# Kernel tuning notes

Measured on AMD Instinct MI355X. Metric: run time of the kernel, lower is better.

## Reference

```python
import jax, jax.numpy as jnp
import numpy as np

CAPACITY_FACTOR = 1.0


def _top1_gate(x2d, wg):
    """GShard-style top-1 switch gate.
    x2d: [S, m], wg: [m, E] -> (l_aux, combine [S,E,C], dispatch [S,E,C])
    """
    S, _ = x2d.shape
    E = wg.shape[1]
    C = int(CAPACITY_FACTOR * S / E)  # expert capacity
    logits = x2d @ wg                              # [S, E]
    gates = jax.nn.softmax(logits, axis=-1)        # [S, E]
    idx = jnp.argmax(gates, axis=-1)               # [S]
    mask = jax.nn.one_hot(idx, E, dtype=jnp.int32) # [S, E]
    loc = jnp.cumsum(mask, axis=0) - 1             # position within each expert
    # load-balancing aux loss
    me = jnp.mean(gates, axis=0)
    ce = jnp.mean(mask.astype(gates.dtype), axis=0)
    l_aux = E * jnp.sum(me * ce)
    # drop tokens over capacity
    mask = mask * (loc < C).astype(jnp.int32)
    gate_s = jnp.sum(gates * mask, axis=-1)        # [S] gate value of kept token
    loc_s = jnp.sum(loc * mask, axis=-1)           # [S] slot index
    loc_oh = jax.nn.one_hot(loc_s, C, dtype=gates.dtype)          # [S, C]
    combine = (gate_s[:, None] * mask.astype(gates.dtype))[:, :, None] * loc_oh[:, None, :]  # [S,E,C]
    dispatch = (combine > 0).astype(gates.dtype)
    return l_aux, combine, dispatch


def setup_inputs() -> dict:
    key = jax.random.key(0)
    k1, k2, k3, k4 = jax.random.split(key, 4)
    s, b, m, E, ffn = 2048, 4, 1024, 8, 4096
    x = jax.random.normal(k1, (s, b, m), dtype=jnp.float32)
    wg = jax.random.normal(k2, (m, E), dtype=jnp.float32) * 0.02
    w1 = jax.random.normal(k3, (E, m, ffn), dtype=jnp.float32) * 0.02
    w2 = jax.random.normal(k4, (E, ffn, m), dtype=jnp.float32) * 0.02
    return {"x": x, "wg": wg, "w1": w1, "w2": w2}


def reference(x, wg, w1, w2):
    # world_size = 1, num_local_experts = E, num_prototypes z = 1
    s, b, m = x.shape
    x2d = x.reshape(-1, m)                          # [S, m]
    l_aux, combine, dispatch = _top1_gate(x2d, wg)  # [S,E,C]
    combine = combine[:, None]                      # [S, z=1, E, C]
    dispatch = dispatch[:, None]
    xr = x2d[:, None, :]                            # [S, z=1, m]
    # dense dispatch: szfc,szm->zfcm
    dispatched = jnp.einsum('szfc,szm->zfcm', dispatch, xr)
    # all-to-all with world_size=1 is identity; reshape to [E, C, m]
    E = w1.shape[0]
    di = dispatched.reshape(E, -1, m)               # [E, C, m]
    # experts: per-expert FFN with ReLU
    h = jax.nn.relu(jnp.einsum('ecm,emh->ech', di, w1))
    eo = jnp.einsum('ech,ehm->ecm', h, w2)          # [E, C, m]
    eo = eo[None]                                   # [z=1, E, C, m]
    out = jnp.einsum('szfc,zfcm->sm', combine, eo)  # [S, m]
    return out.reshape(s, b, m)
```

## Files before the change

### kernel.cpp

```cpp
#include <hip/hip_runtime.h>
#include <hip/hip_bf16.h>


#define NTOK 8192
#define DM   1024
#define NE   8
#define NF   4096
#define CAP  1024

typedef __bf16 bf16x8 __attribute__((ext_vector_type(8)));
typedef float  f32x4  __attribute__((ext_vector_type(4)));

__device__ __forceinline__ unsigned short f2bf(float f) {
    union { float f; unsigned int u; } v; v.f = f;
    unsigned int u = v.u;
    return (unsigned short)((u + 0x7FFFu + ((u >> 16) & 1u)) >> 16);
}

__device__ __forceinline__ void async_cp16(const unsigned short* g, unsigned short* l) {
    __builtin_amdgcn_global_load_lds(
        (const __attribute__((address_space(1))) void*)g,
        (__attribute__((address_space(3))) void*)l, 16, 0, 0);
}

__global__ __launch_bounds__(256) void gate_kernel(
    const float* __restrict__ x, const float* __restrict__ wg,
    int* __restrict__ eid, float* __restrict__ gatev)
{
    int wave = threadIdx.x >> 6;
    int lane = threadIdx.x & 63;
    int t = blockIdx.x * 4 + wave;
    const float* xr = x + (size_t)t * DM;
    float acc[NE];
#pragma unroll
    for (int e = 0; e < NE; ++e) acc[e] = 0.f;
    for (int k = lane; k < DM; k += 64) {
        float xv = xr[k];
        const float4* wr = (const float4*)(wg + k * NE);
        float4 w0 = wr[0], w1 = wr[1];
        acc[0] += xv * w0.x; acc[1] += xv * w0.y;
        acc[2] += xv * w0.z; acc[3] += xv * w0.w;
        acc[4] += xv * w1.x; acc[5] += xv * w1.y;
        acc[6] += xv * w1.z; acc[7] += xv * w1.w;
    }
#pragma unroll
    for (int off = 32; off >= 1; off >>= 1) {
#pragma unroll
        for (int e = 0; e < NE; ++e) acc[e] += __shfl_xor(acc[e], off, 64);
    }
    if (lane == 0) {
        int best = 0; float bm = acc[0];
#pragma unroll
        for (int e = 1; e < NE; ++e) if (acc[e] > bm) { bm = acc[e]; best = e; }
        float ssum = 0.f;
#pragma unroll
        for (int e = 0; e < NE; ++e) ssum += __expf(acc[e] - bm);
        eid[t] = best;
        gatev[t] = 1.0f / ssum;
    }
}

__global__ __launch_bounds__(1024) void scan_kernel(
    const int* __restrict__ eid, int* __restrict__ slot_token)
{
    __shared__ int sc[1024][NE];
    int tid = threadIdx.x;
#pragma unroll
    for (int i = 0; i < 8; ++i) slot_token[tid + i * 1024] = -1;

    int e_loc[8];
    int cnt[NE];
#pragma unroll
    for (int e = 0; e < NE; ++e) cnt[e] = 0;
#pragma unroll
    for (int i = 0; i < 8; ++i) {
        int e = eid[tid * 8 + i];
        e_loc[i] = e;
        cnt[e]++;
    }
#pragma unroll
    for (int e = 0; e < NE; ++e) sc[tid][e] = cnt[e];
    __syncthreads();
    for (int stride = 1; stride < 1024; stride <<= 1) {
        int v[NE];
        if (tid >= stride) {
#pragma unroll
            for (int e = 0; e < NE; ++e) v[e] = sc[tid - stride][e];
        } else {
#pragma unroll
            for (int e = 0; e < NE; ++e) v[e] = 0;
        }
        __syncthreads();
#pragma unroll
        for (int e = 0; e < NE; ++e) sc[tid][e] += v[e];
        __syncthreads();
    }
    int off_[NE];
#pragma unroll
    for (int e = 0; e < NE; ++e) off_[e] = (tid == 0) ? 0 : sc[tid - 1][e];
#pragma unroll
    for (int i = 0; i < 8; ++i) {
        int e = e_loc[i];
        int loc = off_[e]++;
        if (loc < CAP) slot_token[e * CAP + loc] = tid * 8 + i;
    }
}

template<int K, int N>
__global__ __launch_bounds__(256) void convT_kernel(
    const float* __restrict__ W, unsigned short* __restrict__ WT)
{
    __shared__ unsigned short tile[64][66];
    int e = blockIdx.z;
    int k0 = blockIdx.y * 64, n0 = blockIdx.x * 64;
    const float* Wp = W + (size_t)e * K * N;
    unsigned short* WTp = WT + (size_t)e * K * N;
    int tid = threadIdx.x;
    int cn = (tid & 15) * 4;
    int rk = tid >> 4;
#pragma unroll
    for (int i = 0; i < 4; ++i) {
        int k = rk + i * 16;
        float4 v = *(const float4*)(Wp + (size_t)(k0 + k) * N + n0 + cn);
        tile[cn + 0][k] = f2bf(v.x);
        tile[cn + 1][k] = f2bf(v.y);
        tile[cn + 2][k] = f2bf(v.z);
        tile[cn + 3][k] = f2bf(v.w);
    }
    __syncthreads();
    int ck = (tid & 15) * 4;
    int rn = tid >> 4;
#pragma unroll
    for (int i = 0; i < 4; ++i) {
        int n = rn + i * 16;
        ushort4 o;
        o.x = tile[n][ck + 0]; o.y = tile[n][ck + 1];
        o.z = tile[n][ck + 2]; o.w = tile[n][ck + 3];
        *(ushort4*)(WTp + (size_t)(n0 + n) * K + k0 + ck) = o;
    }
}

__global__ __launch_bounds__(256) void gather_kernel(
    const float* __restrict__ x, const int* __restrict__ slot_token,
    unsigned short* __restrict__ Xd)
{
    int slot = blockIdx.x;
    int t = slot_token[slot];
    int c4 = threadIdx.x * 4;
    ushort4 o;
    if (t >= 0) {
        float4 v = *(const float4*)(x + (size_t)t * DM + c4);
        o.x = f2bf(v.x); o.y = f2bf(v.y); o.z = f2bf(v.z); o.w = f2bf(v.w);
    } else {
        o.x = 0; o.y = 0; o.z = 0; o.w = 0;
    }
    *(ushort4*)(Xd + (size_t)slot * DM + c4) = o;
}

template<int K>
__device__ __forceinline__ void gemm_core(
    const unsigned short* __restrict__ Ab, const unsigned short* __restrict__ Bb,
    unsigned short* As, unsigned short* Bs, f32x4 acc[4][4])
{
    int tid = threadIdx.x;
    int wave = tid >> 6, lane = tid & 63;
    int wr = (wave >> 1) * 64;
    int wc = (wave & 1) * 64;
#pragma unroll
    for (int i = 0; i < 4; ++i)
#pragma unroll
        for (int j = 0; j < 4; ++j) acc[i][j] = (f32x4){0.f, 0.f, 0.f, 0.f};

    int srow = (lane >> 2);
    int scol = (lane & 3) * 8;

    for (int kt = 0; kt < K; kt += 32) {
#pragma unroll
        for (int i = 0; i < 2; ++i) {
            int q = wave * 2 + i;
            int row = q * 16 + srow;
            const unsigned short* ga = Ab + (size_t)row * K + kt + scol;
            const unsigned short* gb = Bb + (size_t)row * K + kt + scol;
            async_cp16(ga, As + q * 512);
            async_cp16(gb, Bs + q * 512);
        }
        __syncthreads();
        bf16x8 af[4], bfr[4];
#pragma unroll
        for (int i = 0; i < 4; ++i) {
            int r = wr + i * 16 + (lane & 15);
            af[i] = *(const bf16x8*)(As + r * 32 + (lane >> 4) * 8);
        }
#pragma unroll
        for (int j = 0; j < 4; ++j) {
            int c = wc + j * 16 + (lane & 15);
            bfr[j] = *(const bf16x8*)(Bs + c * 32 + (lane >> 4) * 8);
        }
#pragma unroll
        for (int i = 0; i < 4; ++i)
#pragma unroll
            for (int j = 0; j < 4; ++j)
                acc[i][j] = __builtin_amdgcn_mfma_f32_16x16x32_bf16(af[i], bfr[j], acc[i][j], 0, 0, 0);
        __syncthreads();
    }
}

__global__ __launch_bounds__(256, 2) void gemm1_kernel(
    const unsigned short* __restrict__ Xd, const unsigned short* __restrict__ W1T,
    unsigned short* __restrict__ H)
{
    __shared__ unsigned short As[128 * 32];
    __shared__ unsigned short Bs[128 * 32];
    int e = blockIdx.z;
    const unsigned short* Ab = Xd + ((size_t)e * CAP + blockIdx.y * 128) * DM;
    const unsigned short* Bb = W1T + ((size_t)e * NF + blockIdx.x * 128) * DM;
    f32x4 acc[4][4];
    gemm_core<DM>(Ab, Bb, As, Bs, acc);

    int tid = threadIdx.x, wave = tid >> 6, lane = tid & 63;
    int wr = (wave >> 1) * 64, wc = (wave & 1) * 64;
    size_t Hbase = ((size_t)e * CAP + blockIdx.y * 128) * NF + blockIdx.x * 128;
#pragma unroll
    for (int i = 0; i < 4; ++i) {
#pragma unroll
        for (int j = 0; j < 4; ++j) {
            int col = wc + j * 16 + (lane & 15);
#pragma unroll
            for (int f = 0; f < 4; ++f) {
                int row = wr + i * 16 + (lane >> 4) * 4 + f;
                float v = acc[i][j][f];
                v = v > 0.f ? v : 0.f;
                H[Hbase + (size_t)row * NF + col] = f2bf(v);
            }
        }
    }
}

__global__ __launch_bounds__(256, 2) void gemm2_kernel(
    const unsigned short* __restrict__ H, const unsigned short* __restrict__ W2T,
    const int* __restrict__ slot_token, const float* __restrict__ gatev,
    float* __restrict__ out)
{
    __shared__ unsigned short As[128 * 32];
    __shared__ unsigned short Bs[128 * 32];
    int e = blockIdx.z;
    const unsigned short* Ab = H + ((size_t)e * CAP + blockIdx.y * 128) * NF;
    const unsigned short* Bb = W2T + ((size_t)e * DM + blockIdx.x * 128) * NF;
    f32x4 acc[4][4];
    gemm_core<NF>(Ab, Bb, As, Bs, acc);

    int tid = threadIdx.x, wave = tid >> 6, lane = tid & 63;
    int wr = (wave >> 1) * 64, wc = (wave & 1) * 64;
    int slot0 = e * CAP + blockIdx.y * 128;
#pragma unroll
    for (int i = 0; i < 4; ++i) {
        int rbase = wr + i * 16 + (lane >> 4) * 4;
#pragma unroll
        for (int f = 0; f < 4; ++f) {
            int row = rbase + f;
            int t = slot_token[slot0 + row];
            if (t >= 0) {
                float g = gatev[t];
#pragma unroll
                for (int j = 0; j < 4; ++j) {
                    int col = blockIdx.x * 128 + wc + j * 16 + (lane & 15);
                    out[(size_t)t * DM + col] = acc[i][j][f] * g;
                }
            }
        }
    }
}

extern "C" void kernel_launch(void* const* d_in, const int* in_sizes, int n_in,
                              void* d_out, int out_size, void* d_ws, size_t ws_size,
                              hipStream_t stream)
{
    const float* x  = (const float*)d_in[0];
    const float* wg = (const float*)d_in[1];
    const float* w1 = (const float*)d_in[2];
    const float* w2 = (const float*)d_in[3];
    float* out = (float*)d_out;

    char* ws = (char*)d_ws;
    size_t o = 0;
    auto nxt = [&](size_t b) { size_t r = o; o += (b + 255) & ~(size_t)255; return r; };
    int*   eid        = (int*)  (ws + nxt((size_t)NTOK * 4));
    float* gatev      = (float*)(ws + nxt((size_t)NTOK * 4));
    int*   slot_token = (int*)  (ws + nxt((size_t)NTOK * 4));
    unsigned short* Xd = (unsigned short*)(ws + nxt((size_t)NTOK * DM * 2));
    unsigned short* WT = (unsigned short*)(ws + nxt((size_t)NE * NF * DM * 2));
    unsigned short* Hb = (unsigned short*)(ws + nxt((size_t)NE * CAP * NF * 2));

    gate_kernel<<<NTOK / 4, 256, 0, stream>>>(x, wg, eid, gatev);
    scan_kernel<<<1, 1024, 0, stream>>>(eid, slot_token);
    convT_kernel<DM, NF><<<dim3(NF / 64, DM / 64, NE), 256, 0, stream>>>(w1, WT);
    gather_kernel<<<NTOK, 256, 0, stream>>>(x, slot_token, Xd);
    gemm1_kernel<<<dim3(NF / 128, CAP / 128, NE), 256, 0, stream>>>(Xd, WT, Hb);
    convT_kernel<NF, DM><<<dim3(DM / 64, NF / 64, NE), 256, 0, stream>>>(w2, WT);
    hipMemsetAsync(d_out, 0, (size_t)out_size * sizeof(float), stream);
    gemm2_kernel<<<dim3(DM / 128, CAP / 128, NE), 256, 0, stream>>>(Hb, WT, slot_token, gatev, out);
}
```

Measured before the change: 558.5 us.

## Retile gemm2, stage gemm1 epilogue through LDS, and vectorize gate/scan/gather/transpose

The gemm2 kernel moves to a 128x64 output tile with a K step of 64 and an occupancy hint of 4, launching twice as many blocks so more of the GPU is busy and fewer barriers are paid per K. The gemm1 epilogue writes ReLU'd bf16 into shared memory and then issues coalesced 16-byte stores, replacing scattered 2-byte global writes. The scan kernel switches from a shared-memory Hillis-Steele scan with many block barriers to a wavefront shuffle scan plus per-wave totals. The gate, gather and transpose kernels get wider vector loads and stores. Risks include LDS bank conflicts in the new layouts and a gemm2 tile that reuses B less per load.

```diff
diff --git a/kernel.cpp b/kernel.cpp
--- a/kernel.cpp
+++ b/kernel.cpp
@@ -10,6 +10,7 @@
 
 typedef __bf16 bf16x8 __attribute__((ext_vector_type(8)));
 typedef float  f32x4  __attribute__((ext_vector_type(4)));
+typedef unsigned short us8v __attribute__((ext_vector_type(8)));
 
 __device__ __forceinline__ unsigned short f2bf(float f) {
     union { float f; unsigned int u; } v; v.f = f;
@@ -30,18 +31,24 @@
     int wave = threadIdx.x >> 6;
     int lane = threadIdx.x & 63;
     int t = blockIdx.x * 4 + wave;
-    const float* xr = x + (size_t)t * DM;
+    const float4* xr4 = (const float4*)(x + (size_t)t * DM);
     float acc[NE];
 #pragma unroll
     for (int e = 0; e < NE; ++e) acc[e] = 0.f;
-    for (int k = lane; k < DM; k += 64) {
-        float xv = xr[k];
-        const float4* wr = (const float4*)(wg + k * NE);
-        float4 w0 = wr[0], w1 = wr[1];
-        acc[0] += xv * w0.x; acc[1] += xv * w0.y;
-        acc[2] += xv * w0.z; acc[3] += xv * w0.w;
-        acc[4] += xv * w1.x; acc[5] += xv * w1.y;
-        acc[6] += xv * w1.z; acc[7] += xv * w1.w;
+#pragma unroll
+    for (int it = 0; it < 4; ++it) {
+        int k4 = lane + it * 64;
+        float4 xv = xr4[k4];
+        float xc[4] = {xv.x, xv.y, xv.z, xv.w};
+#pragma unroll
+        for (int c = 0; c < 4; ++c) {
+            const float4* wr = (const float4*)(wg + (size_t)(k4 * 4 + c) * NE);
+            float4 w0 = wr[0], w1 = wr[1];
+            acc[0] += xc[c] * w0.x; acc[1] += xc[c] * w0.y;
+            acc[2] += xc[c] * w0.z; acc[3] += xc[c] * w0.w;
+            acc[4] += xc[c] * w1.x; acc[5] += xc[c] * w1.y;
+            acc[6] += xc[c] * w1.z; acc[7] += xc[c] * w1.w;
+        }
     }
 #pragma unroll
     for (int off = 32; off >= 1; off >>= 1) {
@@ -63,45 +70,49 @@
 __global__ __launch_bounds__(1024) void scan_kernel(
     const int* __restrict__ eid, int* __restrict__ slot_token)
 {
-    __shared__ int sc[1024][NE];
+    __shared__ int wtot[16][NE];
     int tid = threadIdx.x;
+    int lane = tid & 63, wv = tid >> 6;
 #pragma unroll
     for (int i = 0; i < 8; ++i) slot_token[tid + i * 1024] = -1;
 
-    int e_loc[8];
+    int el[8];
     int cnt[NE];
 #pragma unroll
     for (int e = 0; e < NE; ++e) cnt[e] = 0;
 #pragma unroll
     for (int i = 0; i < 8; ++i) {
         int e = eid[tid * 8 + i];
-        e_loc[i] = e;
+        el[i] = e;
         cnt[e]++;
     }
-#pragma unroll
-    for (int e = 0; e < NE; ++e) sc[tid][e] = cnt[e];
+    int incl[NE];
+#pragma unroll
+    for (int e = 0; e < NE; ++e) incl[e] = cnt[e];
+#pragma unroll
+    for (int off = 1; off <= 32; off <<= 1) {
+#pragma unroll
+        for (int e = 0; e < NE; ++e) {
+            int v = __shfl_up(incl[e], off, 64);
+            if (lane >= off) incl[e] += v;
+        }
+    }
+    if (lane == 63) {
+#pragma unroll
+        for (int e = 0; e < NE; ++e) wtot[wv][e] = incl[e];
+    }
     __syncthreads();
-    for (int stride = 1; stride < 1024; stride <<= 1) {
-        int v[NE];
-        if (tid >= stride) {
-#pragma unroll
-            for (int e = 0; e < NE; ++e) v[e] = sc[tid - stride][e];
-        } else {
-#pragma unroll
-            for (int e = 0; e < NE; ++e) v[e] = 0;
-        }
-        __syncthreads();
-#pragma unroll
-        for (int e = 0; e < NE; ++e) sc[tid][e] += v[e];
-        __syncthreads();
-    }
-    int off_[NE];
-#pragma unroll
-    for (int e = 0; e < NE; ++e) off_[e] = (tid == 0) ? 0 : sc[tid - 1][e];
+    int base[NE];
+#pragma unroll
+    for (int e = 0; e < NE; ++e) {
+        int s = 0;
+        for (int w = 0; w < 16; ++w) s += (w < wv) ? wtot[w][e] : 0;
+        base[e] = s + incl[e] - cnt[e];
+    }
 #pragma unroll
     for (int i = 0; i < 8; ++i) {
-        int e = e_loc[i];
-        int loc = off_[e]++;
+        int e = el[i];
+        int loc = base[e]++;
         if (loc < CAP) slot_token[e * CAP + loc] = tid * 8 + i;
     }
 }
@@ -110,7 +121,7 @@
 __global__ __launch_bounds__(256) void convT_kernel(
     const float* __restrict__ W, unsigned short* __restrict__ WT)
 {
-    __shared__ unsigned short tile[64][66];
+    __shared__ unsigned short tile[64][72];
     int e = blockIdx.z;
     int k0 = blockIdx.y * 64, n0 = blockIdx.x * 64;
     const float* Wp = W + (size_t)e * K * N;
@@ -128,15 +139,15 @@
         tile[cn + 3][k] = f2bf(v.w);
     }
     __syncthreads();
-    int ck = (tid & 15) * 4;
-    int rn = tid >> 4;
-#pragma unroll
-    for (int i = 0; i < 4; ++i) {
-        int n = rn + i * 16;
-        ushort4 o;
-        o.x = tile[n][ck + 0]; o.y = tile[n][ck + 1];
-        o.z = tile[n][ck + 2]; o.w = tile[n][ck + 3];
-        *(ushort4*)(WTp + (size_t)(n0 + n) * K + k0 + ck) = o;
+    int ck = (tid & 7) * 8;
+    int rn = tid >> 3;
+#pragma unroll
+    for (int i = 0; i < 2; ++i) {
+        int n = rn + i * 32;
+        us8v o;
+#pragma unroll
+        for (int c = 0; c < 8; ++c) o[c] = tile[n][ck + c];
+        *(us8v*)(WTp + (size_t)(n0 + n) * K + k0 + ck) = o;
     }
 }
 
@@ -144,17 +155,22 @@
     const float* __restrict__ x, const int* __restrict__ slot_token,
     unsigned short* __restrict__ Xd)
 {
-    int slot = blockIdx.x;
+    int tid = threadIdx.x;
+    int local = tid & 127;
+    int slot = blockIdx.x * 2 + (tid >> 7);
     int t = slot_token[slot];
-    int c4 = threadIdx.x * 4;
-    ushort4 o;
+    int c = local * 8;
+    us8v o;
     if (t >= 0) {
-        float4 v = *(const float4*)(x + (size_t)t * DM + c4);
-        o.x = f2bf(v.x); o.y = f2bf(v.y); o.z = f2bf(v.z); o.w = f2bf(v.w);
+        const float4* p = (const float4*)(x + (size_t)t * DM + c);
+        float4 v0 = p[0], v1 = p[1];
+        o[0] = f2bf(v0.x); o[1] = f2bf(v0.y); o[2] = f2bf(v0.z); o[3] = f2bf(v0.w);
+        o[4] = f2bf(v1.x); o[5] = f2bf(v1.y); o[6] = f2bf(v1.z); o[7] = f2bf(v1.w);
     } else {
-        o.x = 0; o.y = 0; o.z = 0; o.w = 0;
-    }
-    *(ushort4*)(Xd + (size_t)slot * DM + c4) = o;
+#pragma unroll
+        for (int c8 = 0; c8 < 8; ++c8) o[c8] = 0;
+    }
+    *(us8v*)(Xd + (size_t)slot * DM + c) = o;
 }
 
 template<int K>
@@ -179,10 +195,8 @@
         for (int i = 0; i < 2; ++i) {
             int q = wave * 2 + i;
             int row = q * 16 + srow;
-            const unsigned short* ga = Ab + (size_t)row * K + kt + scol;
-            const unsigned short* gb = Bb + (size_t)row * K + kt + scol;
-            async_cp16(ga, As + q * 512);
-            async_cp16(gb, Bs + q * 512);
+            async_cp16(Ab + (size_t)row * K + kt + scol, As + q * 512);
+            async_cp16(Bb + (size_t)row * K + kt + scol, Bs + q * 512);
         }
         __syncthreads();
         bf16x8 af[4], bfr[4];
@@ -209,8 +223,9 @@
     const unsigned short* __restrict__ Xd, const unsigned short* __restrict__ W1T,
     unsigned short* __restrict__ H)
 {
-    __shared__ unsigned short As[128 * 32];
-    __shared__ unsigned short Bs[128 * 32];
+    __shared__ unsigned short smem[8192];
+    unsigned short* As = smem;
+    unsigned short* Bs = smem + 4096;
     int e = blockIdx.z;
     const unsigned short* Ab = Xd + ((size_t)e * CAP + blockIdx.y * 128) * DM;
     const unsigned short* Bb = W1T + ((size_t)e * NF + blockIdx.x * 128) * DM;
@@ -218,39 +233,98 @@
     gemm_core<DM>(Ab, Bb, As, Bs, acc);
 
     int tid = threadIdx.x, wave = tid >> 6, lane = tid & 63;
-    int wr = (wave >> 1) * 64, wc = (wave & 1) * 64;
-    size_t Hbase = ((size_t)e * CAP + blockIdx.y * 128) * NF + blockIdx.x * 128;
-#pragma unroll
-    for (int i = 0; i < 4; ++i) {
-#pragma unroll
-        for (int j = 0; j < 4; ++j) {
-            int col = wc + j * 16 + (lane & 15);
-#pragma unroll
-            for (int f = 0; f < 4; ++f) {
-                int row = wr + i * 16 + (lane >> 4) * 4 + f;
-                float v = acc[i][j][f];
-                v = v > 0.f ? v : 0.f;
-                H[Hbase + (size_t)row * NF + col] = f2bf(v);
+    int wc = (wave & 1) * 64;
+    size_t Hrow0 = ((size_t)e * CAP + blockIdx.y * 128) * NF + blockIdx.x * 128;
+    unsigned short* buf = smem;
+#pragma unroll
+    for (int p = 0; p < 2; ++p) {
+        if ((wave >> 1) == p) {
+#pragma unroll
+            for (int i = 0; i < 4; ++i) {
+#pragma unroll
+                for (int j = 0; j < 4; ++j) {
+                    int col = wc + j * 16 + (lane & 15);
+#pragma unroll
+                    for (int f = 0; f < 4; ++f) {
+                        int lr = i * 16 + (lane >> 4) * 4 + f;
+                        float v = acc[i][j][f];
+                        v = v > 0.f ? v : 0.f;
+                        buf[lr * 128 + col] = f2bf(v);
+                    }
+                }
             }
         }
-    }
-}
-
-__global__ __launch_bounds__(256, 2) void gemm2_kernel(
+        __syncthreads();
+#pragma unroll
+        for (int v = 0; v < 4; ++v) {
+            int sidx = tid + v * 256;
+            int r = sidx >> 4, seg = sidx & 15;
+            us8v o = *(const us8v*)(buf + r * 128 + seg * 8);
+            *(us8v*)(H + Hrow0 + (size_t)(p * 64 + r) * NF + seg * 8) = o;
+        }
+        __syncthreads();
+    }
+}
+
+__global__ __launch_bounds__(256, 4) void gemm2_kernel(
     const unsigned short* __restrict__ H, const unsigned short* __restrict__ W2T,
     const int* __restrict__ slot_token, const float* __restrict__ gatev,
     float* __restrict__ out)
 {
-    __shared__ unsigned short As[128 * 32];
-    __shared__ unsigned short Bs[128 * 32];
+    __shared__ unsigned short As[128 * 64];
+    __shared__ unsigned short Bs[64 * 64];
     int e = blockIdx.z;
     const unsigned short* Ab = H + ((size_t)e * CAP + blockIdx.y * 128) * NF;
-    const unsigned short* Bb = W2T + ((size_t)e * DM + blockIdx.x * 128) * NF;
-    f32x4 acc[4][4];
-    gemm_core<NF>(Ab, Bb, As, Bs, acc);
+    const unsigned short* Bb = W2T + ((size_t)e * DM + blockIdx.x * 64) * NF;
 
     int tid = threadIdx.x, wave = tid >> 6, lane = tid & 63;
-    int wr = (wave >> 1) * 64, wc = (wave & 1) * 64;
+    int wr = (wave >> 1) * 64;
+    int wc = (wave & 1) * 32;
+    f32x4 acc[4][2];
+#pragma unroll
+    for (int i = 0; i < 4; ++i)
+#pragma unroll
+        for (int j = 0; j < 2; ++j) acc[i][j] = (f32x4){0.f, 0.f, 0.f, 0.f};
+
+    int srow = lane >> 3;
+    int scol = (lane & 7) * 8;
+
+    for (int kt = 0; kt < NF; kt += 64) {
+#pragma unroll
+        for (int i = 0; i < 4; ++i) {
+            int q = wave * 4 + i;
+            int row = q * 8 + srow;
+            async_cp16(Ab + (size_t)row * NF + kt + scol, As + q * 512);
+        }
+#pragma unroll
+        for (int i = 0; i < 2; ++i) {
+            int q = wave * 2 + i;
+            int row = q * 8 + srow;
+            async_cp16(Bb + (size_t)row * NF + kt + scol, Bs + q * 512);
+        }
+        __syncthreads();
+#pragma unroll
+        for (int h = 0; h < 2; ++h) {
+            bf16x8 af[4], bfr[2];
+#pragma unroll
+            for (int i = 0; i < 4; ++i) {
+                int r = wr + i * 16 + (lane & 15);
+                af[i] = *(const bf16x8*)(As + r * 64 + h * 32 + (lane >> 4) * 8);
+            }
+#pragma unroll
+            for (int j = 0; j < 2; ++j) {
+                int c = wc + j * 16 + (lane & 15);
+                bfr[j] = *(const bf16x8*)(Bs + c * 64 + h * 32 + (lane >> 4) * 8);
+            }
+#pragma unroll
+            for (int i = 0; i < 4; ++i)
+#pragma unroll
+                for (int j = 0; j < 2; ++j)
+                    acc[i][j] = __builtin_amdgcn_mfma_f32_16x16x32_bf16(af[i], bfr[j], acc[i][j], 0, 0, 0);
+        }
+        __syncthreads();
+    }
+
     int slot0 = e * CAP + blockIdx.y * 128;
 #pragma unroll
     for (int i = 0; i < 4; ++i) {
@@ -262,8 +336,8 @@
             if (t >= 0) {
                 float g = gatev[t];
 #pragma unroll
-                for (int j = 0; j < 4; ++j) {
-                    int col = blockIdx.x * 128 + wc + j * 16 + (lane & 15);
+                for (int j = 0; j < 2; ++j) {
+                    int col = blockIdx.x * 64 + wc + j * 16 + (lane & 15);
                     out[(size_t)t * DM + col] = acc[i][j][f] * g;
                 }
             }
@@ -294,9 +368,9 @@
     gate_kernel<<<NTOK / 4, 256, 0, stream>>>(x, wg, eid, gatev);
     scan_kernel<<<1, 1024, 0, stream>>>(eid, slot_token);
     convT_kernel<DM, NF><<<dim3(NF / 64, DM / 64, NE), 256, 0, stream>>>(w1, WT);
-    gather_kernel<<<NTOK, 256, 0, stream>>>(x, slot_token, Xd);
+    gather_kernel<<<NTOK / 2, 256, 0, stream>>>(x, slot_token, Xd);
     gemm1_kernel<<<dim3(NF / 128, CAP / 128, NE), 256, 0, stream>>>(Xd, WT, Hb);
     convT_kernel<NF, DM><<<dim3(DM / 64, NF / 64, NE), 256, 0, stream>>>(w2, WT);
     hipMemsetAsync(d_out, 0, (size_t)out_size * sizeof(float), stream);
-    gemm2_kernel<<<dim3(DM / 128, CAP / 128, NE), 256, 0, stream>>>(Hb, WT, slot_token, gatev, out);
-}
+    gemm2_kernel<<<dim3(DM / 64, CAP / 128, NE), 256, 0, stream>>>(Hb, WT, slot_token, gatev, out);
+}
```

After: 552.2 us. About the same (-1.1%).
